# Kernel tuning notes

Measured on AMD Instinct MI355X. Metric: run time of the kernel, lower is better.

## Reference

```python
import jax, jax.numpy as jnp
import numpy as np

LEVELS = 2
BASE_BLOCK = (16, 16)
MAX_DIST = 8
IMG = (1024, 1024)


def _to_blocks(x, bh, bw):
    # [N,C,H,W] -> [BX,BY,N,C,bh,bw]
    N, C, H, W = x.shape
    BX, BY = H // bh, W // bw
    return x.reshape(N, C, BX, bh, BY, bw).transpose(2, 4, 0, 1, 3, 5)


def _from_blocks(b):
    # [BX,BY,N,C,bh,bw] -> [N,C,H,W]
    BX, BY, N, C, bh, bw = b.shape
    return b.transpose(2, 3, 0, 4, 1, 5).reshape(N, C, BX * bh, BY * bw)


def _level_best(ref_b, tgt_b, centers, d):
    # ref_b/tgt_b: [BX,BY,N,C,bh,bw]; centers: [BX,BY,2] candidate-window centers
    BX, BY = ref_b.shape[:2]
    dr = jnp.arange(-d, d + 1)
    offs = jnp.stack(jnp.meshgrid(dr, dr, indexing='ij'), -1).reshape(-1, 2)  # [K,2] lexicographic (dx,dy)
    hi = jnp.array([BX - 1, BY - 1])

    def step(carry, off):
        cand = centers + off  # [BX,BY,2]
        valid = jnp.all((cand >= 0) & (cand <= hi), axis=-1)
        cc = jnp.clip(cand, 0, hi)
        g = tgt_b[cc[..., 0], cc[..., 1]]  # [BX,BY,N,C,bh,bw]
        cost = jnp.mean(jnp.abs(ref_b - g), axis=(2, 3, 4, 5))  # MAD over N,C,h,w
        return carry, jnp.where(valid, cost, jnp.inf)

    _, costs = jax.lax.scan(step, None, offs)  # [K,BX,BY]
    k = jnp.argmin(costs, axis=0)  # first-min tie-break, deterministic
    return centers + offs[k]  # [BX,BY,2] absolute best target-block indices


def reference(reference_frame, target_frame):
    N, C, H, W = reference_frame.shape
    centers = None
    best = None
    tgt_b = None
    BX = BY = 0
    for level in range(LEVELS):
        s = 2 ** (LEVELS - level - 1)
        bh, bw = BASE_BLOCK[0] * s, BASE_BLOCK[1] * s
        BX, BY = H // bh, W // bw
        d = MAX_DIST // (2 ** level)
        ref_b = _to_blocks(reference_frame, bh, bw)
        tgt_b = _to_blocks(target_frame, bh, bw)
        if level == 0:
            gx, gy = jnp.meshgrid(jnp.arange(BX), jnp.arange(BY), indexing='ij')
            centers = jnp.stack([gx, gy], -1)
        best = _level_best(ref_b, tgt_b, centers, d)
        if level < LEVELS - 1:
            # all 4 children inherit window centered at 2*parent_best
            centers = jnp.repeat(jnp.repeat(2 * best, 2, axis=0), 2, axis=1)
    gx, gy = jnp.meshgrid(jnp.arange(BX), jnp.arange(BY), indexing='ij')
    grid = jnp.stack([gx, gy], -1)
    mv = (best - grid).transpose(2, 0, 1)[None].astype(reference_frame.dtype)
    motion_vectors = jnp.broadcast_to(mv, (N, 2, BX, BY))
    pred_b = tgt_b[best[..., 0], best[..., 1]]  # [BX,BY,N,C,bh,bw]
    predicted_frame = _from_blocks(pred_b)
    return motion_vectors, predicted_frame


def setup_inputs() -> dict:
    key = jax.random.key(0)
    k1, k2 = jax.random.split(key)
    N, C = 4, 3
    H, W = IMG
    reference_frame = jax.random.uniform(k1, (N, C, H, W), dtype=jnp.float32)
    target_frame = jax.random.uniform(k2, (N, C, H, W), dtype=jnp.float32)
    return {"reference_frame": reference_frame, "target_frame": target_frame}
```

## Files before the change

### kernel.cpp

```cpp
#include <hip/hip_runtime.h>

#define IMG_W 1024
#define SLICE 1048576
#define INF_F __builtin_huge_valf()
#define WS_PART_FLOATS (12 * 1024 * 289)

template <int CTRL>
__device__ __forceinline__ float dpp_add_step(float x) {
    int m = __builtin_amdgcn_update_dpp(0, __builtin_bit_cast(int, x), CTRL, 0xf, 0xf, true);
    return x + __builtin_bit_cast(float, m);
}
__device__ __forceinline__ float wave_sum63(float x) {
    x = dpp_add_step<0x111>(x);
    x = dpp_add_step<0x112>(x);
    x = dpp_add_step<0x114>(x);
    x = dpp_add_step<0x118>(x);
    x = dpp_add_step<0x142>(x);
    x = dpp_add_step<0x143>(x);
    return x;
}

__global__ __launch_bounds__(512, 4) void hbma_l0_phase1(const float* __restrict__ ref,
                                                         const float* __restrict__ tgt,
                                                         float* __restrict__ part) {
    const int tx    = blockIdx.x;
    const int byq   = blockIdx.y;
    const int plane = blockIdx.z;
    const int t = threadIdx.x;
    const int lane = t & 63, w = t >> 6;
    const int by0 = byq * 8;
    const int by  = by0 + w;

    __shared__ float tile[16 * 1024];

    const int prow = lane >> 3;
    const int pcol = (lane & 7) << 2;

    const float* tgt_p = tgt + (size_t)plane * SLICE;
    const float* ref_p = ref + (size_t)plane * SLICE;

    for (int batch = 0; batch < 2; ++batch) {
        const int tyBase = (batch == 0) ? (by0 - 8) : by0;
        const int dyLo   = (batch == 0) ? -8 : 0;
        const int dyHi   = (batch == 0) ? -1 : 8;

        __syncthreads();
        for (int idx = t; idx < 16 * 256; idx += 512) {
            const int j  = idx >> 8;
            const int ty = tyBase + j;
            if ((unsigned)ty < 32u) {
                const int ww = idx & 255;
                const int rr = ww >> 3;
                const int cc = (ww & 7) << 2;
                *(float4*)&tile[j * 1024 + rr * 32 + cc] =
                    *(const float4*)(tgt_p + (size_t)(tx * 32 + rr) * IMG_W + ty * 32 + cc);
            }
        }
        __syncthreads();

        for (int dxg = 0; dxg < 5; ++dxg) {
            float4 rf[4][4];
            bool rvalid[4];
            #pragma unroll
            for (int r = 0; r < 4; ++r) {
                const int di = dxg * 4 + r;
                const int bx = tx - (di - 8);
                rvalid[r] = (di <= 16) && ((unsigned)bx < 32u);
                if (rvalid[r]) {
                    const float* rb = ref_p + (size_t)(bx * 32 + prow) * IMG_W + by * 32 + pcol;
                    #pragma unroll
                    for (int i = 0; i < 4; ++i)
                        rf[r][i] = *(const float4*)(rb + (size_t)i * 8 * IMG_W);
                }
            }
            for (int dy = dyLo; dy <= dyHi; ++dy) {
                const int ty = by + dy;
                if ((unsigned)ty >= 32u) continue;
                const int tbase = (ty - tyBase) * 1024 + prow * 32 + pcol;
                float4 tv[4];
                #pragma unroll
                for (int i = 0; i < 4; ++i)
                    tv[i] = *(const float4*)&tile[tbase + i * 256];
                #pragma unroll
                for (int r = 0; r < 4; ++r) {
                    if (!rvalid[r]) continue;
                    float4 a = {0.f, 0.f, 0.f, 0.f};
                    #pragma unroll
                    for (int i = 0; i < 4; ++i) {
                        a.x += __builtin_fabsf(rf[r][i].x - tv[i].x);
                        a.y += __builtin_fabsf(rf[r][i].y - tv[i].y);
                        a.z += __builtin_fabsf(rf[r][i].z - tv[i].z);
                        a.w += __builtin_fabsf(rf[r][i].w - tv[i].w);
                    }
                    const float s = wave_sum63((a.x + a.y) + (a.z + a.w));
                    if (lane == 63) {
                        const int di = dxg * 4 + r;
                        const int bx = tx - (di - 8);
                        part[((size_t)plane * 1024 + bx * 32 + by) * 289 + di * 17 + (dy + 8)] = s;
                    }
                }
            }
        }
    }
}

__global__ __launch_bounds__(64) void hbma_l0_phase2(const float* __restrict__ part,
                                                     int2* __restrict__ best0) {
    const int by = blockIdx.x;
    const int bx = blockIdx.y;
    const int t = threadIdx.x;

    float bc = INF_F; int bk = 1 << 30;
    for (int k = t; k < 289; k += 64) {
        const int dx = k / 17 - 8, dy = k % 17 - 8;
        const int tx = bx + dx,    ty = by + dy;
        if ((unsigned)tx < 32u && (unsigned)ty < 32u) {
            float c = 0.f;
            #pragma unroll
            for (int p = 0; p < 12; ++p)
                c += part[((size_t)p * 1024 + bx * 32 + by) * 289 + k];
            if (c < bc) { bc = c; bk = k; }
        }
    }
    #pragma unroll
    for (int o = 32; o > 0; o >>= 1) {
        const float oc = __shfl_down(bc, o, 64);
        const int   ok = __shfl_down(bk, o, 64);
        if (oc < bc || (oc == bc && ok < bk)) { bc = oc; bk = ok; }
    }
    if (t == 0) best0[bx * 32 + by] = make_int2(bx + bk / 17 - 8, by + bk % 17 - 8);
}

__global__ __launch_bounds__(256) void hbma_l1(const float* __restrict__ ref,
                                               const float* __restrict__ tgt,
                                               const int2* __restrict__ best0,
                                               float* __restrict__ out) {
    const int pby = blockIdx.x;
    const int pbx = blockIdx.y;
    const int t = threadIdx.x;
    const int lane = t & 63, w = t >> 6;

    __shared__ float partials[4][81][4];
    __shared__ int2 sbest[4];

    const int2 pb = best0[pbx * 32 + pby];
    const int cx = 2 * pb.x, cy = 2 * pb.y;

    int off[3];
    #pragma unroll
    for (int i = 0; i < 3; ++i) {
        const int e4 = t + 256 * i;
        const int nc = e4 >> 6;
        const int ww = e4 & 63;
        off[i] = nc * SLICE + (ww >> 2) * IMG_W + ((ww & 3) << 2);
    }
    int cbase[4];
    float4 rf[4][3];
    #pragma unroll
    for (int c = 0; c < 4; ++c) {
        const int bx = 2 * pbx + (c >> 1), by = 2 * pby + (c & 1);
        cbase[c] = (bx * 16) * IMG_W + by * 16;
        #pragma unroll
        for (int i = 0; i < 3; ++i)
            rf[c][i] = *(const float4*)(ref + cbase[c] + off[i]);
    }

    for (int k = 0; k < 81; ++k) {
        const int tx = cx + k / 9 - 4;
        const int ty = cy + k % 9 - 4;
        if ((unsigned)tx < 64u && (unsigned)ty < 64u) {
            const float* tb = tgt + (tx * 16) * IMG_W + ty * 16;
            float4 tv[3];
            #pragma unroll
            for (int i = 0; i < 3; ++i) tv[i] = *(const float4*)(tb + off[i]);
            #pragma unroll
            for (int c = 0; c < 4; ++c) {
                float4 a = {0.f, 0.f, 0.f, 0.f};
                #pragma unroll
                for (int i = 0; i < 3; ++i) {
                    a.x += __builtin_fabsf(rf[c][i].x - tv[i].x);
                    a.y += __builtin_fabsf(rf[c][i].y - tv[i].y);
                    a.z += __builtin_fabsf(rf[c][i].z - tv[i].z);
                    a.w += __builtin_fabsf(rf[c][i].w - tv[i].w);
                }
                const float s = wave_sum63((a.x + a.y) + (a.z + a.w));
                if (lane == 63) partials[c][k][w] = s;
            }
        } else if (lane == 63) {
            #pragma unroll
            for (int c = 0; c < 4; ++c) partials[c][k][w] = INF_F;
        }
    }
    __syncthreads();

    {
        const int c = w;
        float bc = INF_F; int bk = 1 << 30;
        for (int k = lane; k < 81; k += 64) {
            const float4 p4 = *(const float4*)&partials[c][k][0];
            const float cost = (p4.x + p4.y) + (p4.z + p4.w);
            if (cost < bc) { bc = cost; bk = k; }
        }
        #pragma unroll
        for (int o = 32; o > 0; o >>= 1) {
            const float oc = __shfl_down(bc, o, 64);
            const int   ok = __shfl_down(bk, o, 64);
            if (oc < bc || (oc == bc && ok < bk)) { bc = oc; bk = ok; }
        }
        if (lane == 0) sbest[c] = make_int2(cx + bk / 9 - 4, cy + bk % 9 - 4);
    }
    __syncthreads();

    if (t < 32) {
        const int c = t >> 3, n = (t >> 1) & 3, ch = t & 1;
        const int bx = 2 * pbx + (c >> 1), by = 2 * pby + (c & 1);
        const int2 fb = sbest[c];
        out[((n * 2 + ch) * 64 + bx) * 64 + by] = (ch == 0) ? (float)(fb.x - bx) : (float)(fb.y - by);
    }

    float* pred = out + 32768;
    #pragma unroll
    for (int c = 0; c < 4; ++c) {
        const int2 fb = sbest[c];
        const float* sb = tgt + (fb.x * 16) * IMG_W + fb.y * 16;
        float* db = pred + cbase[c];
        #pragma unroll
        for (int i = 0; i < 3; ++i)
            *(float4*)(db + off[i]) = *(const float4*)(sb + off[i]);
    }
}

extern "C" void kernel_launch(void* const* d_in, const int* in_sizes, int n_in,
                              void* d_out, int out_size, void* d_ws, size_t ws_size,
                              hipStream_t stream) {
    const float* ref = (const float*)d_in[0];
    const float* tgt = (const float*)d_in[1];
    float* out = (float*)d_out;

    float* part  = (float*)d_ws;
    int2*  best0 = (int2*)((char*)d_ws + (size_t)WS_PART_FLOATS * 4);

    hbma_l0_phase1<<<dim3(32, 4, 12), 512, 0, stream>>>(ref, tgt, part);
    hbma_l0_phase2<<<dim3(32, 32), 64, 0, stream>>>(part, best0);
    hbma_l1<<<dim3(32, 32), 256, 0, stream>>>(ref, tgt, best0, out);
}
```

Before: 512.3 us.

## Accumulate level-0 costs across planes in registers and fold argmin into level-1

The level-0 kernel now loops over all 12 planes inside each block, keeping per-lane partial SADs for 5 dx by 17 dy candidates in registers. It does one wave reduction per candidate at the end instead of one per plane, and writes a single cost array instead of 12 per-plane partials. The separate argmin kernel is removed and its work moves into the start of the level-1 kernel. Target tiles are staged with global_load_lds direct-to-LDS copies. The change trades a large register footprint (85 accumulators plus 20 float4 ref values) and a different grid split along dx for less workspace traffic, fewer reductions and one fewer launch.

```diff
diff --git a/kernel.cpp b/kernel.cpp
--- a/kernel.cpp
+++ b/kernel.cpp
@@ -3,7 +3,6 @@
 #define IMG_W 1024
 #define SLICE 1048576
 #define INF_F __builtin_huge_valf()
-#define WS_PART_FLOATS (12 * 1024 * 289)
 
 template <int CTRL>
 __device__ __forceinline__ float dpp_add_step(float x) {
@@ -20,120 +19,109 @@
     return x;
 }
 
-__global__ __launch_bounds__(512, 4) void hbma_l0_phase1(const float* __restrict__ ref,
-                                                         const float* __restrict__ tgt,
-                                                         float* __restrict__ part) {
-    const int tx    = blockIdx.x;
-    const int byq   = blockIdx.y;
-    const int plane = blockIdx.z;
-    const int t = threadIdx.x;
-    const int lane = t & 63, w = t >> 6;
-    const int by0 = byq * 8;
-    const int by  = by0 + w;
-
-    __shared__ float tile[16 * 1024];
-
-    const int prow = lane >> 3;
-    const int pcol = (lane & 7) << 2;
-
-    const float* tgt_p = tgt + (size_t)plane * SLICE;
-    const float* ref_p = ref + (size_t)plane * SLICE;
-
-    for (int batch = 0; batch < 2; ++batch) {
-        const int tyBase = (batch == 0) ? (by0 - 8) : by0;
-        const int dyLo   = (batch == 0) ? -8 : 0;
-        const int dyHi   = (batch == 0) ? -1 : 8;
+typedef const float __attribute__((address_space(1))) gfloat;
+typedef float __attribute__((address_space(3))) sfloat;
+
+__global__ __launch_bounds__(256, 2) void hbma_l0(const float* __restrict__ ref,
+                                                  const float* __restrict__ tgt,
+                                                  float* __restrict__ cost) {
+    const int tx  = blockIdx.x;
+    const int byo = blockIdx.y;
+    const int dxq = blockIdx.z;
+    const int di0 = dxq * 4;
+    const int ndi = (dxq == 3) ? 5 : 4;
+    const int t = threadIdx.x, lane = t & 63, w = t >> 6;
+    const int by = byo * 4 + w;
+    const int prow = lane >> 3, pcol = (lane & 7) << 2;
+    const int ty0 = byo * 4 - 8;
+
+    __shared__ float tile[20 * 1024];
+
+    float acc[5][17];
+    #pragma unroll
+    for (int d = 0; d < 5; ++d)
+        #pragma unroll
+        for (int y = 0; y < 17; ++y) acc[d][y] = 0.f;
+
+    bool rvalid[5]; int bxv[5];
+    #pragma unroll
+    for (int d = 0; d < 5; ++d) {
+        const int bx = tx - (di0 + d - 8);
+        bxv[d] = bx;
+        rvalid[d] = (d < ndi) && ((unsigned)bx < 32u);
+    }
+
+    const int srr = t >> 3, scc = (t & 7) << 2;
+
+    for (int plane = 0; plane < 12; ++plane) {
+        const float* tgt_p = tgt + (size_t)plane * SLICE;
+        const float* ref_p = ref + (size_t)plane * SLICE;
 
         __syncthreads();
-        for (int idx = t; idx < 16 * 256; idx += 512) {
-            const int j  = idx >> 8;
-            const int ty = tyBase + j;
+        #pragma unroll
+        for (int i = 0; i < 20; ++i) {
+            const int ty = ty0 + i;
             if ((unsigned)ty < 32u) {
-                const int ww = idx & 255;
-                const int rr = ww >> 3;
-                const int cc = (ww & 7) << 2;
-                *(float4*)&tile[j * 1024 + rr * 32 + cc] =
-                    *(const float4*)(tgt_p + (size_t)(tx * 32 + rr) * IMG_W + ty * 32 + cc);
+                __builtin_amdgcn_global_load_lds(
+                    (gfloat*)(tgt_p + (size_t)(tx * 32 + srr) * IMG_W + ty * 32 + scc),
+                    (sfloat*)&tile[(i * 256 + t) * 4], 16, 0, 0);
             }
         }
         __syncthreads();
 
-        for (int dxg = 0; dxg < 5; ++dxg) {
-            float4 rf[4][4];
-            bool rvalid[4];
-            #pragma unroll
-            for (int r = 0; r < 4; ++r) {
-                const int di = dxg * 4 + r;
-                const int bx = tx - (di - 8);
-                rvalid[r] = (di <= 16) && ((unsigned)bx < 32u);
-                if (rvalid[r]) {
-                    const float* rb = ref_p + (size_t)(bx * 32 + prow) * IMG_W + by * 32 + pcol;
-                    #pragma unroll
-                    for (int i = 0; i < 4; ++i)
-                        rf[r][i] = *(const float4*)(rb + (size_t)i * 8 * IMG_W);
+        float4 rf[5][4];
+        #pragma unroll
+        for (int d = 0; d < 5; ++d)
+            if (rvalid[d]) {
+                const float* rb = ref_p + (size_t)(bxv[d] * 32 + prow) * IMG_W + by * 32 + pcol;
+                #pragma unroll
+                for (int i = 0; i < 4; ++i)
+                    rf[d][i] = *(const float4*)(rb + (size_t)i * 8 * IMG_W);
+            }
+
+        #pragma unroll
+        for (int yi = 0; yi < 17; ++yi) {
+            const int ty = by + yi - 8;
+            if ((unsigned)ty < 32u) {
+                const int tb = (ty - ty0) * 1024 + prow * 32 + pcol;
+                float4 tv[4];
+                #pragma unroll
+                for (int i = 0; i < 4; ++i) tv[i] = *(const float4*)&tile[tb + i * 256];
+                #pragma unroll
+                for (int d = 0; d < 5; ++d)
+                    if (rvalid[d]) {
+                        float4 a = {0.f, 0.f, 0.f, 0.f};
+                        #pragma unroll
+                        for (int i = 0; i < 4; ++i) {
+                            a.x += __builtin_fabsf(rf[d][i].x - tv[i].x);
+                            a.y += __builtin_fabsf(rf[d][i].y - tv[i].y);
+                            a.z += __builtin_fabsf(rf[d][i].z - tv[i].z);
+                            a.w += __builtin_fabsf(rf[d][i].w - tv[i].w);
+                        }
+                        acc[d][yi] += (a.x + a.y) + (a.z + a.w);
+                    }
+            }
+        }
+    }
+
+    #pragma unroll
+    for (int d = 0; d < 5; ++d)
+        if (rvalid[d]) {
+            #pragma unroll
+            for (int yi = 0; yi < 17; ++yi) {
+                const int ty = by + yi - 8;
+                if ((unsigned)ty < 32u) {
+                    const float s = wave_sum63(acc[d][yi]);
+                    if (lane == 63)
+                        cost[((size_t)bxv[d] * 32 + by) * 289 + (size_t)(di0 + d) * 17 + yi] = s;
                 }
             }
-            for (int dy = dyLo; dy <= dyHi; ++dy) {
-                const int ty = by + dy;
-                if ((unsigned)ty >= 32u) continue;
-                const int tbase = (ty - tyBase) * 1024 + prow * 32 + pcol;
-                float4 tv[4];
-                #pragma unroll
-                for (int i = 0; i < 4; ++i)
-                    tv[i] = *(const float4*)&tile[tbase + i * 256];
-                #pragma unroll
-                for (int r = 0; r < 4; ++r) {
-                    if (!rvalid[r]) continue;
-                    float4 a = {0.f, 0.f, 0.f, 0.f};
-                    #pragma unroll
-                    for (int i = 0; i < 4; ++i) {
-                        a.x += __builtin_fabsf(rf[r][i].x - tv[i].x);
-                        a.y += __builtin_fabsf(rf[r][i].y - tv[i].y);
-                        a.z += __builtin_fabsf(rf[r][i].z - tv[i].z);
-                        a.w += __builtin_fabsf(rf[r][i].w - tv[i].w);
-                    }
-                    const float s = wave_sum63((a.x + a.y) + (a.z + a.w));
-                    if (lane == 63) {
-                        const int di = dxg * 4 + r;
-                        const int bx = tx - (di - 8);
-                        part[((size_t)plane * 1024 + bx * 32 + by) * 289 + di * 17 + (dy + 8)] = s;
-                    }
-                }
-            }
-        }
-    }
-}
-
-__global__ __launch_bounds__(64) void hbma_l0_phase2(const float* __restrict__ part,
-                                                     int2* __restrict__ best0) {
-    const int by = blockIdx.x;
-    const int bx = blockIdx.y;
-    const int t = threadIdx.x;
-
-    float bc = INF_F; int bk = 1 << 30;
-    for (int k = t; k < 289; k += 64) {
-        const int dx = k / 17 - 8, dy = k % 17 - 8;
-        const int tx = bx + dx,    ty = by + dy;
-        if ((unsigned)tx < 32u && (unsigned)ty < 32u) {
-            float c = 0.f;
-            #pragma unroll
-            for (int p = 0; p < 12; ++p)
-                c += part[((size_t)p * 1024 + bx * 32 + by) * 289 + k];
-            if (c < bc) { bc = c; bk = k; }
-        }
-    }
-    #pragma unroll
-    for (int o = 32; o > 0; o >>= 1) {
-        const float oc = __shfl_down(bc, o, 64);
-        const int   ok = __shfl_down(bk, o, 64);
-        if (oc < bc || (oc == bc && ok < bk)) { bc = oc; bk = ok; }
-    }
-    if (t == 0) best0[bx * 32 + by] = make_int2(bx + bk / 17 - 8, by + bk % 17 - 8);
+        }
 }
 
 __global__ __launch_bounds__(256) void hbma_l1(const float* __restrict__ ref,
                                                const float* __restrict__ tgt,
-                                               const int2* __restrict__ best0,
+                                               const float* __restrict__ cost,
                                                float* __restrict__ out) {
     const int pby = blockIdx.x;
     const int pbx = blockIdx.y;
@@ -142,9 +130,36 @@
 
     __shared__ float partials[4][81][4];
     __shared__ int2 sbest[4];
-
-    const int2 pb = best0[pbx * 32 + pby];
-    const int cx = 2 * pb.x, cy = 2 * pb.y;
+    __shared__ float pm_c[4];
+    __shared__ int pm_k[4];
+
+    float bc = INF_F; int bk = 1 << 30;
+    {
+        const float* crow = cost + ((size_t)pbx * 32 + pby) * 289;
+        for (int k = t; k < 289; k += 256) {
+            const int dx = k / 17 - 8, dy = k % 17 - 8;
+            if ((unsigned)(pbx + dx) < 32u && (unsigned)(pby + dy) < 32u) {
+                const float c = crow[k];
+                if (c < bc) { bc = c; bk = k; }
+            }
+        }
+        #pragma unroll
+        for (int o = 32; o > 0; o >>= 1) {
+            const float oc = __shfl_down(bc, o, 64);
+            const int   ok = __shfl_down(bk, o, 64);
+            if (oc < bc || (oc == bc && ok < bk)) { bc = oc; bk = ok; }
+        }
+        if (lane == 0) { pm_c[w] = bc; pm_k[w] = bk; }
+        __syncthreads();
+        bc = pm_c[0]; bk = pm_k[0];
+        #pragma unroll
+        for (int j = 1; j < 4; ++j) {
+            const float oc = pm_c[j]; const int ok = pm_k[j];
+            if (oc < bc || (oc == bc && ok < bk)) { bc = oc; bk = ok; }
+        }
+    }
+    const int cx = 2 * (pbx + bk / 17 - 8);
+    const int cy = 2 * (pby + bk % 17 - 8);
 
     int off[3];
     #pragma unroll
@@ -195,19 +210,19 @@
 
     {
         const int c = w;
-        float bc = INF_F; int bk = 1 << 30;
+        float cbc = INF_F; int cbk = 1 << 30;
         for (int k = lane; k < 81; k += 64) {
             const float4 p4 = *(const float4*)&partials[c][k][0];
-            const float cost = (p4.x + p4.y) + (p4.z + p4.w);
-            if (cost < bc) { bc = cost; bk = k; }
+            const float cst = (p4.x + p4.y) + (p4.z + p4.w);
+            if (cst < cbc) { cbc = cst; cbk = k; }
         }
         #pragma unroll
         for (int o = 32; o > 0; o >>= 1) {
-            const float oc = __shfl_down(bc, o, 64);
-            const int   ok = __shfl_down(bk, o, 64);
-            if (oc < bc || (oc == bc && ok < bk)) { bc = oc; bk = ok; }
-        }
-        if (lane == 0) sbest[c] = make_int2(cx + bk / 9 - 4, cy + bk % 9 - 4);
+            const float oc = __shfl_down(cbc, o, 64);
+            const int   ok = __shfl_down(cbk, o, 64);
+            if (oc < cbc || (oc == cbc && ok < cbk)) { cbc = oc; cbk = ok; }
+        }
+        if (lane == 0) sbest[c] = make_int2(cx + cbk / 9 - 4, cy + cbk % 9 - 4);
     }
     __syncthreads();
 
@@ -237,10 +252,8 @@
     const float* tgt = (const float*)d_in[1];
     float* out = (float*)d_out;
 
-    float* part  = (float*)d_ws;
-    int2*  best0 = (int2*)((char*)d_ws + (size_t)WS_PART_FLOATS * 4);
-
-    hbma_l0_phase1<<<dim3(32, 4, 12), 512, 0, stream>>>(ref, tgt, part);
-    hbma_l0_phase2<<<dim3(32, 32), 64, 0, stream>>>(part, best0);
-    hbma_l1<<<dim3(32, 32), 256, 0, stream>>>(ref, tgt, best0, out);
-}
+    float* cost = (float*)d_ws;
+
+    hbma_l0<<<dim3(32, 8, 4), 256, 0, stream>>>(ref, tgt, cost);
+    hbma_l1<<<dim3(32, 32), 256, 0, stream>>>(ref, tgt, cost, out);
+}
```

Result: slower. 947.0 us (+84.9%).

## Fuse level-0 argmin into level-1 kernel, remap blocks, double-buffer target loads

Applied to the files above, without the earlier changes.

Removes the separate phase-2 kernel and has each level-1 workgroup reduce the twelve level-0 partial cost planes for its own parent block, using a cross-wave shared-memory argmin. The block index is remapped to a different traversal order, likely to improve cache locality of target reads. The 81-candidate loop is software-pipelined with two register buffers so the next candidate's loads are issued before the current one is computed. In exchange the fused kernel does redundant-free but serialized extra work per block, needs an added barrier, and carries more register pressure.

```diff
diff --git a/kernel.cpp b/kernel.cpp
--- a/kernel.cpp
+++ b/kernel.cpp
@@ -104,47 +104,51 @@
     }
 }
 
-__global__ __launch_bounds__(64) void hbma_l0_phase2(const float* __restrict__ part,
-                                                     int2* __restrict__ best0) {
-    const int by = blockIdx.x;
-    const int bx = blockIdx.y;
-    const int t = threadIdx.x;
-
-    float bc = INF_F; int bk = 1 << 30;
-    for (int k = t; k < 289; k += 64) {
-        const int dx = k / 17 - 8, dy = k % 17 - 8;
-        const int tx = bx + dx,    ty = by + dy;
-        if ((unsigned)tx < 32u && (unsigned)ty < 32u) {
-            float c = 0.f;
-            #pragma unroll
-            for (int p = 0; p < 12; ++p)
-                c += part[((size_t)p * 1024 + bx * 32 + by) * 289 + k];
-            if (c < bc) { bc = c; bk = k; }
-        }
-    }
-    #pragma unroll
-    for (int o = 32; o > 0; o >>= 1) {
-        const float oc = __shfl_down(bc, o, 64);
-        const int   ok = __shfl_down(bk, o, 64);
-        if (oc < bc || (oc == bc && ok < bk)) { bc = oc; bk = ok; }
-    }
-    if (t == 0) best0[bx * 32 + by] = make_int2(bx + bk / 17 - 8, by + bk % 17 - 8);
-}
-
 __global__ __launch_bounds__(256) void hbma_l1(const float* __restrict__ ref,
                                                const float* __restrict__ tgt,
-                                               const int2* __restrict__ best0,
+                                               const float* __restrict__ part,
                                                float* __restrict__ out) {
-    const int pby = blockIdx.x;
-    const int pbx = blockIdx.y;
+    const int pid = blockIdx.y * 32 + blockIdx.x;
+    const int pbx = ((pid & 7) << 2) + ((pid >> 3) >> 5);
+    const int pby = (pid >> 3) & 31;
     const int t = threadIdx.x;
     const int lane = t & 63, w = t >> 6;
 
     __shared__ float partials[4][81][4];
     __shared__ int2 sbest[4];
-
-    const int2 pb = best0[pbx * 32 + pby];
-    const int cx = 2 * pb.x, cy = 2 * pb.y;
+    __shared__ float pm_c[4];
+    __shared__ int pm_k[4];
+
+    float bc = INF_F; int bk = 1 << 30;
+    {
+        const size_t blk = (size_t)pbx * 32 + pby;
+        for (int k = t; k < 289; k += 256) {
+            const int dx = k / 17 - 8, dy = k % 17 - 8;
+            if ((unsigned)(pbx + dx) < 32u && (unsigned)(pby + dy) < 32u) {
+                float c = 0.f;
+                #pragma unroll
+                for (int p = 0; p < 12; ++p)
+                    c += part[((size_t)p * 1024 + blk) * 289 + k];
+                if (c < bc) { bc = c; bk = k; }
+            }
+        }
+        #pragma unroll
+        for (int o = 32; o > 0; o >>= 1) {
+            const float oc = __shfl_down(bc, o, 64);
+            const int   ok = __shfl_down(bk, o, 64);
+            if (oc < bc || (oc == bc && ok < bk)) { bc = oc; bk = ok; }
+        }
+        if (lane == 0) { pm_c[w] = bc; pm_k[w] = bk; }
+        __syncthreads();
+        bc = pm_c[0]; bk = pm_k[0];
+        #pragma unroll
+        for (int j = 1; j < 4; ++j) {
+            const float oc = pm_c[j]; const int ok = pm_k[j];
+            if (oc < bc || (oc == bc && ok < bk)) { bc = oc; bk = ok; }
+        }
+    }
+    const int cx = 2 * (pbx + bk / 17 - 8);
+    const int cy = 2 * (pby + bk % 17 - 8);
 
     int off[3];
     #pragma unroll
@@ -165,14 +169,20 @@
             rf[c][i] = *(const float4*)(ref + cbase[c] + off[i]);
     }
 
-    for (int k = 0; k < 81; ++k) {
-        const int tx = cx + k / 9 - 4;
-        const int ty = cy + k % 9 - 4;
-        if ((unsigned)tx < 64u && (unsigned)ty < 64u) {
-            const float* tb = tgt + (tx * 16) * IMG_W + ty * 16;
-            float4 tv[3];
+    auto issue = [&](int k, float4 (&tv)[3]) -> bool {
+        const int ttx = cx + k / 9 - 4;
+        const int tty = cy + k % 9 - 4;
+        const bool valid = ((unsigned)ttx < 64u) && ((unsigned)tty < 64u);
+        if (valid) {
+            const float* tb = tgt + (ttx * 16) * IMG_W + tty * 16;
             #pragma unroll
             for (int i = 0; i < 3; ++i) tv[i] = *(const float4*)(tb + off[i]);
+        }
+        return valid;
+    };
+    auto compute = [&](int k, const float4 (&tv)[3], bool valid) {
+        if (k >= 81) return;
+        if (valid) {
             #pragma unroll
             for (int c = 0; c < 4; ++c) {
                 float4 a = {0.f, 0.f, 0.f, 0.f};
@@ -190,24 +200,34 @@
             #pragma unroll
             for (int c = 0; c < 4; ++c) partials[c][k][w] = INF_F;
         }
+    };
+
+    float4 tvA[3], tvB[3];
+    bool vA = issue(0, tvA);
+    for (int k = 0; k < 81; k += 2) {
+        const bool vB = (k + 1 < 81) && issue(k + 1, tvB);
+        compute(k, tvA, vA);
+        const bool vA2 = (k + 2 < 81) && issue(k + 2, tvA);
+        compute(k + 1, tvB, vB);
+        vA = vA2;
     }
     __syncthreads();
 
     {
         const int c = w;
-        float bc = INF_F; int bk = 1 << 30;
+        float cbc = INF_F; int cbk = 1 << 30;
         for (int k = lane; k < 81; k += 64) {
             const float4 p4 = *(const float4*)&partials[c][k][0];
-            const float cost = (p4.x + p4.y) + (p4.z + p4.w);
-            if (cost < bc) { bc = cost; bk = k; }
+            const float cst = (p4.x + p4.y) + (p4.z + p4.w);
+            if (cst < cbc) { cbc = cst; cbk = k; }
         }
         #pragma unroll
         for (int o = 32; o > 0; o >>= 1) {
-            const float oc = __shfl_down(bc, o, 64);
-            const int   ok = __shfl_down(bk, o, 64);
-            if (oc < bc || (oc == bc && ok < bk)) { bc = oc; bk = ok; }
-        }
-        if (lane == 0) sbest[c] = make_int2(cx + bk / 9 - 4, cy + bk % 9 - 4);
+            const float oc = __shfl_down(cbc, o, 64);
+            const int   ok = __shfl_down(cbk, o, 64);
+            if (oc < cbc || (oc == cbc && ok < cbk)) { cbc = oc; cbk = ok; }
+        }
+        if (lane == 0) sbest[c] = make_int2(cx + cbk / 9 - 4, cy + cbk % 9 - 4);
     }
     __syncthreads();
 
@@ -237,10 +257,8 @@
     const float* tgt = (const float*)d_in[1];
     float* out = (float*)d_out;
 
-    float* part  = (float*)d_ws;
-    int2*  best0 = (int2*)((char*)d_ws + (size_t)WS_PART_FLOATS * 4);
+    float* part = (float*)d_ws;
 
     hbma_l0_phase1<<<dim3(32, 4, 12), 512, 0, stream>>>(ref, tgt, part);
-    hbma_l0_phase2<<<dim3(32, 32), 64, 0, stream>>>(part, best0);
-    hbma_l1<<<dim3(32, 32), 256, 0, stream>>>(ref, tgt, best0, out);
-}
+    hbma_l1<<<dim3(32, 32), 256, 0, stream>>>(ref, tgt, part, out);
+}
```

Result: faster. 488.4 us (-4.7%).
